# Performance work log

Measured on AMD Instinct MI355X. Metric: run time of the kernel, lower is better.

## Reference

```python
import jax, jax.numpy as jnp
import numpy as np

MAX_N = 32        # mixture degree N
N_PTS = 16384     # number of scalar inputs
INIT_DECAY = 1.0


def setup_inputs() -> dict:
    key = jax.random.key(0)
    k1, _ = jax.random.split(key)
    # inputs assumed elementwise in [-1, 1]
    xs = jax.random.uniform(k1, (N_PTS,), dtype=jnp.float32, minval=-1.0, maxval=1.0)
    # learned logits param, init logits[n] = -n * init_decay (as in __init__)
    logits = -INIT_DECAY * jnp.arange(MAX_N + 1, dtype=jnp.float32)
    return {"xs": xs, "logits": logits}


def _psi(xs, logits, max_n):
    """psi(x) = concat_n sqrt(w_n) * phi_n(x); shape (P, 2*max_n+1).

    phi_0 = [1]; phi_n = [T_n(x), sqrt(1-x^2) * U_{n-1}(x)] for n>=1.
    Single linear-pass recurrence instead of per-degree recompute.
    """
    w = jax.nn.softmax(logits)          # (max_n+1,)
    sw = jnp.sqrt(w)
    xc = jnp.clip(xs, -1.0, 1.0)        # (P,)
    s = jnp.sqrt(jnp.clip(1.0 - xc * xc, 0.0))
    P = xs.shape[0]

    # T_0..T_max_n and U_0..U_max_n via one shared recurrence (fixed small loop)
    Ts = [jnp.ones_like(xc), xc]
    Us = [jnp.ones_like(xc), 2.0 * xc]
    for _ in range(2, max_n + 1):
        Ts.append(2.0 * xc * Ts[-1] - Ts[-2])
        Us.append(2.0 * xc * Us[-1] - Us[-2])
    T = jnp.stack(Ts, axis=-1)          # (P, max_n+1)
    U = jnp.stack(Us, axis=-1)          # (P, max_n+1)

    Tn = T[:, 1:]                       # T_1..T_N            (P, max_n)
    Un = U[:, :max_n]                   # U_0..U_{N-1}        (P, max_n)
    # interleave per degree: [T_n, s * U_{n-1}], weighted by sqrt(w_n)
    pair = jnp.stack([Tn, s[:, None] * Un], axis=-1)   # (P, max_n, 2)
    pair = pair * sw[1:][None, :, None]
    head = sw[0] * jnp.ones((P, 1), dtype=xs.dtype)    # sqrt(w_0) * phi_0
    return jnp.concatenate([head, pair.reshape(P, 2 * max_n)], axis=-1)


def reference(xs, logits):
    """gram(xs) = psi(xs) @ psi(xs)^T, shape (P, P)."""
    psi = _psi(xs, logits, MAX_N)       # (P, 2*MAX_N+1)
    return psi @ psi.T
```

## Files before the change

kernel.cpp:

```cpp
#include <hip/hip_runtime.h>
#include <hip/hip_bf16.h>
#include <math.h>

#define MAXN    32
#define NPTS    16384
#define NPSI    65
#define RSTRIDE 104
#define BTA     64
#define BTB     128
#define NROWS   (BTA + BTB)
#define NCHUNK  (NROWS * RSTRIDE * 2 / 1024)

typedef __attribute__((ext_vector_type(8))) short  bf16x8;
typedef __attribute__((ext_vector_type(4))) float  f32x4;

__device__ inline ushort f2bf(float f) {
    union { float f; unsigned u; } v; v.f = f;
    unsigned u = v.u;
    u += 0x7FFFu + ((u >> 16) & 1u);
    return (ushort)(u >> 16);
}

__global__ __launch_bounds__(256) void psi_kernel(
    const float* __restrict__ xs, const float* __restrict__ logits,
    ushort* __restrict__ psi)
{
    int pt = blockIdx.x * blockDim.x + threadIdx.x;
    if (pt >= NPTS) return;

    float x = xs[pt];
    x = fminf(1.0f, fmaxf(-1.0f, x));
    float s = sqrtf(fmaxf(0.0f, 1.0f - x * x));

    float m = -3.4e38f;
    #pragma unroll
    for (int n = 0; n <= MAXN; ++n) m = fmaxf(m, logits[n]);
    float sum = 0.0f;
    #pragma unroll
    for (int n = 0; n <= MAXN; ++n) sum += __expf(logits[n] - m);
    float inv = 1.0f / sum;

    ushort tmp[RSTRIDE];
    tmp[0] = f2bf(sqrtf(__expf(logits[0] - m) * inv));
    float Tm1 = 1.0f, T = x;
    float Um1 = 1.0f, U = 2.0f * x;
    float tx = 2.0f * x;
    #pragma unroll
    for (int n = 1; n <= MAXN; ++n) {
        float swn = sqrtf(__expf(logits[n] - m) * inv);
        tmp[2 * n - 1] = f2bf(swn * T);
        tmp[2 * n]     = f2bf(swn * (s * Um1));
        float Tn = tx * T - Tm1; Tm1 = T; T = Tn;
        float Un = tx * U - Um1; Um1 = U; U = Un;
    }
    #pragma unroll
    for (int k = NPSI; k < RSTRIDE; ++k) tmp[k] = 0;

    unsigned long long* dst = (unsigned long long*)(psi + (size_t)pt * RSTRIDE);
    const unsigned long long* src = (const unsigned long long*)tmp;
    #pragma unroll
    for (int k = 0; k < RSTRIDE / 4; ++k) dst[k] = src[k];
}

__device__ inline void load_lds16(const void* g, void* l) {
    __builtin_amdgcn_global_load_lds(
        (const __attribute__((address_space(1))) unsigned*)g,
        (__attribute__((address_space(3))) unsigned*)l, 16, 0, 0);
}

__global__ __launch_bounds__(256) void gram_kernel(
    const ushort* __restrict__ psi, float* __restrict__ out)
{
    __shared__ ushort lds[NROWS * RSTRIDE];

    const int tid  = threadIdx.x;
    const int w    = tid >> 6;
    const int lane = tid & 63;
    const int bi   = blockIdx.y;
    const int bj   = blockIdx.x;

    {
        const char* gA = (const char*)(psi + (size_t)bi * BTA * RSTRIDE);
        const char* gB = (const char*)(psi + (size_t)bj * BTB * RSTRIDE);
        char* lbase = (char*)lds;
        for (int q = w; q < NCHUNK; q += 4) {
            const char* src = (q < 13) ? (gA + q * 1024) : (gB + (q - 13) * 1024);
            load_lds16(src + lane * 16, lbase + q * 1024);
        }
    }
    __syncthreads();

    const int lr = lane & 15;
    const int lk = (lane >> 4) * 8;
    const int cq = (lane >> 4) * 4;

    const ushort* aBase = lds + (w * 16 + lr) * RSTRIDE;
    const ushort* bBase = lds + (BTA + lr) * RSTRIDE;

    f32x4 acc[8];
    #pragma unroll
    for (int ct = 0; ct < 8; ++ct) acc[ct] = (f32x4){0.f, 0.f, 0.f, 0.f};

    #pragma unroll
    for (int ks = 0; ks < 3; ++ks) {
        bf16x8 a = *(const bf16x8*)(aBase + ks * 32 + lk);
        #pragma unroll
        for (int ct = 0; ct < 8; ++ct) {
            bf16x8 b = *(const bf16x8*)(bBase + ct * 16 * RSTRIDE + ks * 32 + lk);
            acc[ct] = __builtin_amdgcn_mfma_f32_16x16x32_bf16(b, a, acc[ct], 0, 0, 0);
        }
    }

    __syncthreads();
    float* ldsF = (float*)lds;
    {
        const int row = w * 16 + lr;
        const int rx  = (row & 7) << 2;
        #pragma unroll
        for (int ct = 0; ct < 8; ++ct) {
            int col = (cq + ct * 16) ^ rx;
            *(f32x4*)(ldsF + row * BTB + col) = acc[ct];
        }
    }
    __syncthreads();

    {
        const int rsub = tid >> 5;
        const int col  = (tid & 31) * 4;
        #pragma unroll
        for (int p = 0; p < 8; ++p) {
            int row  = p * 8 + rsub;
            int colr = col ^ ((row & 7) << 2);
            f32x4 v = *(const f32x4*)(ldsF + row * BTB + colr);
            float* dst = out + (size_t)(bi * BTA + row) * NPTS + (size_t)bj * BTB + col;
            *(f32x4*)dst = v;
        }
    }
}

extern "C" void kernel_launch(void* const* d_in, const int* in_sizes, int n_in,
                              void* d_out, int out_size, void* d_ws, size_t ws_size,
                              hipStream_t stream) {
    const float* xs     = (const float*)d_in[0];
    const float* logits = (const float*)d_in[1];
    float* out          = (float*)d_out;
    ushort* psi         = (ushort*)d_ws;

    psi_kernel<<<NPTS / 256, 256, 0, stream>>>(xs, logits, psi);

    dim3 grid(NPTS / BTB, NPTS / BTA);
    gram_kernel<<<grid, 256, 0, stream>>>(psi, out);
}
```

Before: 190.7 us.

## Fold constant w0 term into accumulator init and shrink psi rows to 64

The constant head column of psi contributes w0 to every Gram entry, so it is dropped from the stored rows and added by initialising the accumulators to w0. Rows shrink from a padded 104 to exactly 64 bf16 values, which cuts the K loop from three MFMA steps to two and reduces psi traffic and LDS footprint. The psi writer stores rows in an XOR-swizzled 16-byte order so LDS reads avoid bank conflicts, and the gram kernel asks for five blocks per CU. The output write of the 1 GB result likely dominates, so the gain is bounded by store bandwidth.

```diff
diff --git a/kernel.cpp b/kernel.cpp
--- a/kernel.cpp
+++ b/kernel.cpp
@@ -4,15 +4,15 @@
 
 #define MAXN    32
 #define NPTS    16384
-#define NPSI    65
-#define RSTRIDE 104
+#define RSTRIDE 64
 #define BTA     64
 #define BTB     128
-#define NROWS   (BTA + BTB)
-#define NCHUNK  (NROWS * RSTRIDE * 2 / 1024)
+#define NCHUNK  ((BTA + BTB) * RSTRIDE * 2 / 1024)
+#define W0_OFF  (NPTS * RSTRIDE)
 
-typedef __attribute__((ext_vector_type(8))) short  bf16x8;
-typedef __attribute__((ext_vector_type(4))) float  f32x4;
+typedef __attribute__((ext_vector_type(8))) short         bf16x8;
+typedef __attribute__((ext_vector_type(4))) float         f32x4;
+typedef __attribute__((ext_vector_type(4))) unsigned int  u32x4;
 
 __device__ inline ushort f2bf(float f) {
     union { float f; unsigned u; } v; v.f = f;
@@ -23,7 +23,7 @@
 
 __global__ __launch_bounds__(256) void psi_kernel(
     const float* __restrict__ xs, const float* __restrict__ logits,
-    ushort* __restrict__ psi)
+    ushort* __restrict__ psi, float* __restrict__ w0scr)
 {
     int pt = blockIdx.x * blockDim.x + threadIdx.x;
     if (pt >= NPTS) return;
@@ -40,26 +40,26 @@
     for (int n = 0; n <= MAXN; ++n) sum += __expf(logits[n] - m);
     float inv = 1.0f / sum;
 
+    if (pt == 0) w0scr[0] = __expf(logits[0] - m) * inv;
+
     ushort tmp[RSTRIDE];
-    tmp[0] = f2bf(sqrtf(__expf(logits[0] - m) * inv));
     float Tm1 = 1.0f, T = x;
     float Um1 = 1.0f, U = 2.0f * x;
     float tx = 2.0f * x;
     #pragma unroll
     for (int n = 1; n <= MAXN; ++n) {
         float swn = sqrtf(__expf(logits[n] - m) * inv);
-        tmp[2 * n - 1] = f2bf(swn * T);
-        tmp[2 * n]     = f2bf(swn * (s * Um1));
+        tmp[2 * n - 2] = f2bf(swn * T);
+        tmp[2 * n - 1] = f2bf(swn * (s * Um1));
         float Tn = tx * T - Tm1; Tm1 = T; T = Tn;
         float Un = tx * U - Um1; Um1 = U; U = Un;
     }
+
+    u32x4* dst = (u32x4*)(psi + (size_t)pt * RSTRIDE);
+    const u32x4* src = (const u32x4*)tmp;
+    const int rx = pt & 7;
     #pragma unroll
-    for (int k = NPSI; k < RSTRIDE; ++k) tmp[k] = 0;
-
-    unsigned long long* dst = (unsigned long long*)(psi + (size_t)pt * RSTRIDE);
-    const unsigned long long* src = (const unsigned long long*)tmp;
-    #pragma unroll
-    for (int k = 0; k < RSTRIDE / 4; ++k) dst[k] = src[k];
+    for (int j = 0; j < 8; ++j) dst[j ^ rx] = src[j];
 }
 
 __device__ inline void load_lds16(const void* g, void* l) {
@@ -68,10 +68,11 @@
         (__attribute__((address_space(3))) unsigned*)l, 16, 0, 0);
 }
 
-__global__ __launch_bounds__(256) void gram_kernel(
-    const ushort* __restrict__ psi, float* __restrict__ out)
+__global__ __launch_bounds__(256, 5) void gram_kernel(
+    const ushort* __restrict__ psi, const float* __restrict__ w0scr,
+    float* __restrict__ out)
 {
-    __shared__ ushort lds[NROWS * RSTRIDE];
+    __shared__ float ldsF[BTA * BTB];
 
     const int tid  = threadIdx.x;
     const int w    = tid >> 6;
@@ -79,46 +80,49 @@
     const int bi   = blockIdx.y;
     const int bj   = blockIdx.x;
 
+    const float w0 = w0scr[0];
+
     {
         const char* gA = (const char*)(psi + (size_t)bi * BTA * RSTRIDE);
         const char* gB = (const char*)(psi + (size_t)bj * BTB * RSTRIDE);
-        char* lbase = (char*)lds;
+        char* lbase = (char*)ldsF;
         for (int q = w; q < NCHUNK; q += 4) {
-            const char* src = (q < 13) ? (gA + q * 1024) : (gB + (q - 13) * 1024);
+            const char* src = (q < 8) ? (gA + q * 1024) : (gB + (q - 8) * 1024);
             load_lds16(src + lane * 16, lbase + q * 1024);
         }
     }
     __syncthreads();
 
     const int lr = lane & 15;
-    const int lk = (lane >> 4) * 8;
-    const int cq = (lane >> 4) * 4;
+    const int lh = lane >> 4;
+    const int cq = lh * 4;
 
-    const ushort* aBase = lds + (w * 16 + lr) * RSTRIDE;
-    const ushort* bBase = lds + (BTA + lr) * RSTRIDE;
+    const char* aRow   = (const char*)ldsF + (w * 16 + lr) * 128;
+    const char* bPanel = (const char*)ldsF + 8192;
 
     f32x4 acc[8];
     #pragma unroll
-    for (int ct = 0; ct < 8; ++ct) acc[ct] = (f32x4){0.f, 0.f, 0.f, 0.f};
+    for (int ct = 0; ct < 8; ++ct) acc[ct] = (f32x4){w0, w0, w0, w0};
 
     #pragma unroll
-    for (int ks = 0; ks < 3; ++ks) {
-        bf16x8 a = *(const bf16x8*)(aBase + ks * 32 + lk);
+    for (int ks = 0; ks < 2; ++ks) {
+        const int slot = (ks * 4 + lh);
+        bf16x8 a = *(const bf16x8*)(aRow + ((slot ^ (lr & 7)) * 16));
         #pragma unroll
         for (int ct = 0; ct < 8; ++ct) {
-            bf16x8 b = *(const bf16x8*)(bBase + ct * 16 * RSTRIDE + ks * 32 + lk);
+            const char* bRow = bPanel + (ct * 16 + lr) * 128;
+            bf16x8 b = *(const bf16x8*)(bRow + ((slot ^ (lr & 7)) * 16));
             acc[ct] = __builtin_amdgcn_mfma_f32_16x16x32_bf16(b, a, acc[ct], 0, 0, 0);
         }
     }
 
     __syncthreads();
-    float* ldsF = (float*)lds;
     {
         const int row = w * 16 + lr;
-        const int rx  = (row & 7) << 2;
+        const int rxe = (row & 7) << 2;
         #pragma unroll
         for (int ct = 0; ct < 8; ++ct) {
-            int col = (cq + ct * 16) ^ rx;
+            int col = (cq + ct * 16) ^ rxe;
             *(f32x4*)(ldsF + row * BTB + col) = acc[ct];
         }
     }
@@ -145,9 +149,10 @@
     const float* logits = (const float*)d_in[1];
     float* out          = (float*)d_out;
     ushort* psi         = (ushort*)d_ws;
+    float*  w0scr       = (float*)((char*)d_ws + (size_t)W0_OFF * 2);
 
-    psi_kernel<<<NPTS / 256, 256, 0, stream>>>(xs, logits, psi);
+    psi_kernel<<<NPTS / 256, 256, 0, stream>>>(xs, logits, psi, w0scr);
 
     dim3 grid(NPTS / BTB, NPTS / BTA);
-    gram_kernel<<<grid, 256, 0, stream>>>(psi, out);
+    gram_kernel<<<grid, 256, 0, stream>>>(psi, w0scr, out);
 }
```

New measurement: 200.4 us. +5.1%, slower.
